# Kernel tuning notes

Hardware: AMD Instinct MI355X
Metric: run time of the kernel (lower is better)

## Reference

```python
import jax, jax.numpy as jnp
import numpy as np

H = 1024
NH = 16
DH = H // NH
EPS = 1e-12


def _heads(x):
    # [B,T,H] -> [B,NH,T,DH]
    B, T, _ = x.shape
    return x.reshape(B, T, NH, DH).transpose(0, 2, 1, 3)


def _layernorm(x, g, b):
    mu = jnp.mean(x, axis=-1, keepdims=True)
    var = jnp.mean(jnp.square(x - mu), axis=-1, keepdims=True)
    return (x - mu) * jax.lax.rsqrt(var + EPS) * g + b


def setup_inputs() -> dict:
    key = jax.random.key(0)
    ks = jax.random.split(key, 24)
    B, Tw, Te = 4, 1024, 128
    s = 0.02
    inp = {
        "word_hidden_states": jax.random.normal(ks[0], (B, Tw, H), jnp.float32),
        "entity_hidden_states": jax.random.normal(ks[1], (B, Te, H), jnp.float32),
        "attention_mask": jnp.zeros((B, 1, 1, Tw + Te), jnp.float32),
        "query_pos": jax.random.normal(ks[2], (B, Te, H), jnp.float32),
    }
    names = ["Wq", "Wk", "Wv", "Weq", "Wek", "Wev", "Wo", "Weo"]
    for i, n in enumerate(names):
        inp[n] = jax.random.normal(ks[3 + i], (H, H), jnp.float32) * s
        inp["b" + n[1:]] = jnp.zeros((H,), jnp.float32)
    inp["ln_g"] = jnp.ones((H,), jnp.float32)
    inp["ln_b"] = jnp.zeros((H,), jnp.float32)
    inp["eln_g"] = jnp.ones((H,), jnp.float32)
    inp["eln_b"] = jnp.zeros((H,), jnp.float32)
    return inp


def reference(word_hidden_states, entity_hidden_states, attention_mask, query_pos,
              Wq, bq, Wk, bk, Wv, bv, Weq, beq, Wek, bek, Wev, bev,
              Wo, bo, Weo, beo, ln_g, ln_b, eln_g, eln_b):
    Tw = word_hidden_states.shape[1]
    pos_ent = (entity_hidden_states + query_pos) * 0.5

    # per-stream projections (entity stream has its own e2w projections)
    qw = _heads(word_hidden_states @ Wq + bq)      # [B,NH,Tw,DH]
    qe = _heads(pos_ent @ Weq + beq)               # [B,NH,Te,DH]
    kw = _heads(word_hidden_states @ Wk + bk)
    ke = _heads(pos_ent @ Wek + bek)
    vw = _heads(word_hidden_states @ Wv + bv)
    ve = _heads(entity_hidden_states @ Wev + bev)  # value uses raw entity states

    q = jnp.concatenate([qw, qe], axis=2)          # [B,NH,T,DH]
    k = jnp.concatenate([kw, ke], axis=2)
    v = jnp.concatenate([vw, ve], axis=2)

    scores = jnp.einsum("bhqd,bhkd->bhqk", q, k) / np.sqrt(DH).astype(np.float32)
    scores = scores + attention_mask
    probs = jax.nn.softmax(scores, axis=-1)
    ctx = jnp.einsum("bhqk,bhkd->bhqd", probs, v)  # [B,NH,T,DH]
    B, _, T, _ = ctx.shape
    ctx = ctx.transpose(0, 2, 1, 3).reshape(B, T, H)

    word_self = ctx[:, :Tw, :]
    ent_self = ctx[:, Tw:, :]

    word_out = _layernorm(word_self @ Wo + bo + word_hidden_states, ln_g, ln_b)
    ent_out = _layernorm(ent_self @ Weo + beo + entity_hidden_states, eln_g, eln_b)
    return (word_out, ent_out)
```

## Files before the change

### kernel.cpp

```cpp
#include <hip/hip_runtime.h>
#include <math.h>

#define H_DIM 1024
#define NHEAD 16
#define DHEAD 64
#define T_W 1024
#define T_E 128
#define T_T 1152
#define BATCH 4

typedef __attribute__((ext_vector_type(8))) short s8b;
typedef __attribute__((ext_vector_type(4))) short s4b;
typedef __attribute__((ext_vector_type(4))) float f32x4;

#define LOG2E 1.44269504088896f

__device__ __forceinline__ unsigned short f2bf(float f) {
    unsigned int u = __float_as_uint(f);
    u = (u + 0x7fffu + ((u >> 16) & 1u)) >> 16;
    return (unsigned short)u;
}

__device__ __forceinline__ unsigned int pk_bf16(float a, float b) {
#if __has_builtin(__builtin_amdgcn_cvt_pk_bf16_f32)
    typedef __bf16 bf2 __attribute__((ext_vector_type(2)));
    bf2 r = __builtin_amdgcn_cvt_pk_bf16_f32(a, b);
    return __builtin_bit_cast(unsigned int, r);
#else
    return (unsigned int)f2bf(a) | ((unsigned int)f2bf(b) << 16);
#endif
}

__device__ __forceinline__ float exp2f_fast(float x) {
#if __has_builtin(__builtin_amdgcn_exp2f)
    return __builtin_amdgcn_exp2f(x);
#else
    return exp2f(x);
#endif
}

__device__ __forceinline__ void gld_lds16(const void* g, void* l) {
    __builtin_amdgcn_global_load_lds(
        (const __attribute__((address_space(1))) unsigned int*)g,
        (__attribute__((address_space(3))) unsigned int*)l, 16, 0, 0);
}

struct WPtrs { const float* w[8]; };
__global__ __launch_bounds__(256) void k_prep2(
    const float* __restrict__ word, const float* __restrict__ ent,
    const float* __restrict__ qp, const float* __restrict__ mask,
    unsigned short* __restrict__ word_bf, unsigned short* __restrict__ pe_bf,
    unsigned short* __restrict__ ent_bf, float* __restrict__ mask2,
    WPtrs ws, unsigned short* __restrict__ Wt)
{
    const int bid = blockIdx.x;
    if (bid < 4096) {
        int i = bid * 256 + threadIdx.x;
        float4 v = ((const float4*)word)[i];
        *(uint2*)(word_bf + (size_t)i * 4) =
            make_uint2(pk_bf16(v.x, v.y), pk_bf16(v.z, v.w));
    } else if (bid < 4608) {
        int i = (bid - 4096) * 256 + threadIdx.x;
        float4 a = ((const float4*)ent)[i];
        float4 b = ((const float4*)qp)[i];
        *(uint2*)(ent_bf + (size_t)i * 4) =
            make_uint2(pk_bf16(a.x, a.y), pk_bf16(a.z, a.w));
        *(uint2*)(pe_bf + (size_t)i * 4) =
            make_uint2(pk_bf16((a.x + b.x) * 0.5f, (a.y + b.y) * 0.5f),
                       pk_bf16((a.z + b.z) * 0.5f, (a.w + b.w) * 0.5f));
    } else if (bid < 4626) {
        int i = (bid - 4608) * 256 + threadIdx.x;
        if (i < BATCH * T_T) mask2[i] = mask[i] * LOG2E;
    } else {
        __shared__ float tile[32][33];
        const int id = bid - 4626;
        const int z = id >> 10, rem = id & 1023;
        const int kb = (rem >> 5) * 32, nb = (rem & 31) * 32;
        const float* src = ws.w[z];
        unsigned short* dst = Wt + (size_t)z * H_DIM * H_DIM;
        const int tx = threadIdx.x & 31, ty = threadIdx.x >> 5;
        #pragma unroll
        for (int i = 0; i < 4; i++)
            tile[ty * 4 + i][tx] = src[(size_t)(kb + ty * 4 + i) * H_DIM + nb + tx];
        __syncthreads();
        #pragma unroll
        for (int i = 0; i < 4; i++)
            dst[(size_t)(nb + ty * 4 + i) * H_DIM + kb + tx] =
                f2bf(tile[tx][ty * 4 + i]);
    }
}

struct B6 { const float* b[6]; };
struct O3p { void* o[3]; };


#define STAGE_GEMM(k0, base)                                                     \
    {                                                                            \
        gld_lds16(gA + (k0), &sm[(base) + t * 8]);                               \
        gld_lds16(gA + (size_t)32 * H_DIM + (k0), &sm[(base) + 2048 + t * 8]);   \
        gld_lds16(gB + (k0), &sm[(base) + 4096 + t * 8]);                        \
        gld_lds16(gB + (size_t)32 * H_DIM + (k0), &sm[(base) + 6144 + t * 8]);   \
        gld_lds16(gB + (size_t)64 * H_DIM + (k0), &sm[(base) + 8192 + t * 8]);   \
        gld_lds16(gB + (size_t)96 * H_DIM + (k0), &sm[(base) + 10240 + t * 8]);  \
    }

#define GEMM_KLOOP                                                               \
    STAGE_GEMM(0, 0)                                                             \
    int base = 0;                                                                \
    for (int k0 = 0; k0 < H_DIM; k0 += 64) {                                     \
        __builtin_amdgcn_s_barrier();                    \
        if (k0 + 64 < H_DIM) {                                                   \
            STAGE_GEMM(k0 + 64, base ^ 12288)                                    \
            asm volatile("s_waitcnt vmcnt(6)" ::: "memory");                     \
        } else {                                                                 \
            asm volatile("s_waitcnt vmcnt(0)" ::: "memory");                     \
        }                                                                        \
        __builtin_amdgcn_s_barrier();                  \
        __builtin_amdgcn_sched_barrier(0);                                       \
        _Pragma("unroll")                                                        \
        for (int kk = 0; kk < 2; kk++) {                                         \
            s8b af[2], bfr[4];                                                   \
            _Pragma("unroll")                                                    \
            for (int mt = 0; mt < 2; mt++) {                                     \
                const int r = wm * 32 + mt * 16 + col;                           \
                af[mt] = *(const s8b*)&sm[base + r * 64 +                        \
                                          (((kk * 4 + quad) ^ (r & 7)) * 8)];    \
            }                                                                    \
            _Pragma("unroll")                                                    \
            for (int nt = 0; nt < 4; nt++) {                                     \
                const int r = wn * 64 + nt * 16 + col;                           \
                bfr[nt] = *(const s8b*)&sm[base + 4096 + r * 64 +                \
                                           (((kk * 4 + quad) ^ (r & 7)) * 8)];   \
            }                                                                    \
            __builtin_amdgcn_s_setprio(1);                                       \
            _Pragma("unroll")                                                    \
            for (int mt = 0; mt < 2; mt++)                                       \
                _Pragma("unroll")                                                \
                for (int nt = 0; nt < 4; nt++)                                   \
                    acc[mt][nt] = __builtin_amdgcn_mfma_f32_16x16x32_bf16(       \
                        af[mt], bfr[nt], acc[mt][nt], 0, 0, 0);                  \
            __builtin_amdgcn_s_setprio(0);                                       \
        }                                                                        \
        base ^= 12288;                                                           \
    }

__global__ __launch_bounds__(256) void k_proj(
    const unsigned short* __restrict__ word_bf,
    const unsigned short* __restrict__ pe_bf,
    const unsigned short* __restrict__ ent_bf,
    const unsigned short* __restrict__ Wtbase, B6 biases, O3p outs)
{
    const int z = blockIdx.z;
    const bool isw = blockIdx.y < 64;
    const int Tseq = isw ? T_W : T_E;
    const int toff = isw ? 0 : T_W;
    const int m0 = (isw ? blockIdx.y : (blockIdx.y - 64)) * 64;
    const unsigned short* A = isw ? word_bf : (z == 2 ? ent_bf : pe_bf);
    const int wi = (isw ? 0 : 3) + z;
    const unsigned short* B = Wtbase + (size_t)wi * H_DIM * H_DIM;
    const float* bias = biases.b[wi];
    void* outp = outs.o[z];

    __shared__ unsigned short sm[24576];
    const int t = threadIdx.x;
    const int w = t >> 6, lane = t & 63;
    const int col = lane & 15, quad = lane >> 4;
    const int n0 = blockIdx.x * 128;
    const int wm = w & 1, wn = w >> 1;

    f32x4 acc[2][4] = {};

    const int rs = t >> 3;
    const int gch = (t & 7) ^ (rs & 7);
    const unsigned short* gA = A + (size_t)(m0 + rs) * H_DIM + gch * 8;
    const unsigned short* gB = B + (size_t)(n0 + rs) * H_DIM + gch * 8;

    GEMM_KLOOP

    #pragma unroll
    for (int mt = 0; mt < 2; mt++) {
        const int mg = m0 + wm * 32 + mt * 16 + quad * 4;
        const int b = mg / Tseq, tt = toff + (mg % Tseq);
        #pragma unroll
        for (int nt = 0; nt < 4; nt++) {
            const int ng = n0 + wn * 64 + nt * 16 + col;
            f32x4 c = acc[mt][nt];
            const float bn = bias[ng];
            if (z < 2) {
                unsigned short* out = (unsigned short*)outp;
                #pragma unroll
                for (int r = 0; r < 4; r++)
                    out[((size_t)b * T_T + tt + r) * H_DIM + ng] = f2bf(c[r] + bn);
            } else {
                unsigned short* out = (unsigned short*)outp;
                *(uint2*)(out + ((size_t)b * H_DIM + ng) * T_T + tt) =
                    make_uint2(pk_bf16(c[0] + bn, c[1] + bn),
                               pk_bf16(c[2] + bn, c[3] + bn));
            }
        }
    }
}

__global__ __launch_bounds__(256) void k_gemm_out(
    const unsigned short* __restrict__ ctx,
    const unsigned short* __restrict__ Wt_o, const unsigned short* __restrict__ Wt_eo,
    const float* __restrict__ bo, const float* __restrict__ beo,
    const float* __restrict__ word, const float* __restrict__ ent,
    float* __restrict__ out_word, float* __restrict__ out_ent)
{
    const int blk = blockIdx.x;
    const bool is_word = blk < 512;
    const int lb = is_word ? blk : blk - 512;
    const int m0 = (lb >> 3) * 64, n0 = (lb & 7) * 128;
    const unsigned short* B = is_word ? Wt_o : Wt_eo;
    const float* bias = is_word ? bo : beo;
    const float* resid = is_word ? word : ent;
    float* out = is_word ? out_word : out_ent;
    const int Tseq = is_word ? T_W : T_E;
    const int toff = is_word ? 0 : T_W;

    __shared__ unsigned short sm[24576];
    const int t = threadIdx.x;
    const int w = t >> 6, lane = t & 63;
    const int col = lane & 15, quad = lane >> 4;
    const int wm = w & 1, wn = w >> 1;

    f32x4 acc[2][4] = {};

    const int rs = t >> 3;
    const int gch = (t & 7) ^ (rs & 7);
    const size_t arow = (size_t)(m0 / Tseq) * T_T + toff + (m0 % Tseq) + rs;
    const unsigned short* gA = ctx + arow * H_DIM + gch * 8;
    const unsigned short* gB = B + (size_t)(n0 + rs) * H_DIM + gch * 8;

    GEMM_KLOOP

    #pragma unroll
    for (int mt = 0; mt < 2; mt++) {
        const int mg = m0 + wm * 32 + mt * 16 + quad * 4;
        #pragma unroll
        for (int nt = 0; nt < 4; nt++) {
            const int ng = n0 + wn * 64 + nt * 16 + col;
            f32x4 c = acc[mt][nt];
            const float bn = bias[ng];
            #pragma unroll
            for (int r = 0; r < 4; r++) {
                const size_t idx = (size_t)(mg + r) * H_DIM + ng;
                out[idx] = c[r] + bn + resid[idx];
            }
        }
    }
}

__global__ __launch_bounds__(512) void k_attn(
    const unsigned short* __restrict__ q, const unsigned short* __restrict__ k,
    const unsigned short* __restrict__ vt, const float* __restrict__ mask2,
    unsigned short* __restrict__ ctx)
{
    const int tid = threadIdx.x;
    const int w = tid >> 6, lane = tid & 63;
    const int col = lane & 15, quad = lane >> 4;
    const int bid = blockIdx.x;
    const int bh = ((bid & 7) << 3) | ((bid >> 3) & 7);
    const int q0 = (bid >> 6) * 128 + w * 16;
    const int b = bh >> 4, h = bh & 15;

    __shared__ unsigned short sK[2][64 * 64];
    __shared__ unsigned short sV[2][64 * 64];
    __shared__ __align__(16) unsigned short sP[8][16 * 64];
    unsigned short* sp = &sP[w][0];

    const unsigned short* qp = q + ((size_t)b * T_T + q0) * H_DIM + h * DHEAD;
    const unsigned short* kp = k + (size_t)b * T_T * H_DIM + h * DHEAD;
    const unsigned short* vp = vt + ((size_t)b * H_DIM + h * DHEAD) * T_T;
    const float* mp = mask2 + (size_t)b * T_T;

    const s8b qf0 = *(const s8b*)(qp + (size_t)col * H_DIM + quad * 8);
    const s8b qf1 = *(const s8b*)(qp + (size_t)col * H_DIM + 32 + quad * 8);

    const int rA = tid >> 3;
    const int cA = (tid & 7) ^ (rA & 7);

    const float SC2 = 0.125f * LOG2E;

    f32x4 O[4] = {};
    float l_part = 0.f;

    #define PREFETCH(J0, BUF)                                                        \
        {                                                                            \
            gld_lds16(kp + (size_t)((J0) + rA) * H_DIM + cA * 8,                     \
                      &sK[BUF][0] + tid * 8);                                        \
            gld_lds16(vp + (size_t)rA * T_T + (J0) + cA * 8,                         \
                      &sV[BUF][0] + tid * 8);                                        \
        }

    PREFETCH(0, 0)
    for (int it = 0; it < 18; it++) {
        const int j0 = it * 64;
        __builtin_amdgcn_s_barrier();
        float4 mrow[4];
        #pragma unroll
        for (int kt = 0; kt < 4; kt++)
            mrow[kt] = *(const float4*)(mp + j0 + kt * 16 + quad * 4);
        __builtin_amdgcn_sched_barrier(0);
        if (it < 17) {
            PREFETCH(j0 + 64, (it + 1) & 1)
            asm volatile("s_waitcnt vmcnt(6)" ::: "memory");
        } else {
            asm volatile("s_waitcnt vmcnt(4)" ::: "memory");
        }
        __builtin_amdgcn_s_barrier();
        __builtin_amdgcn_sched_barrier(0);

        const unsigned short* K0 = &sK[it & 1][0];
        const unsigned short* V0 = &sV[it & 1][0];

        float p[16];
        #pragma unroll
        for (int kt = 0; kt < 4; kt++) {
            const int rk = kt * 16 + col;
            const int csw = quad ^ (rk & 7);
            s8b k0f = *(const s8b*)(K0 + rk * 64 + csw * 8);
            s8b k1f = *(const s8b*)(K0 + rk * 64 + (csw ^ 4) * 8);
            f32x4 z = {0.f, 0.f, 0.f, 0.f};
            __builtin_amdgcn_s_setprio(1);
            z = __builtin_amdgcn_mfma_f32_16x16x32_bf16(k0f, qf0, z, 0, 0, 0);
            z = __builtin_amdgcn_mfma_f32_16x16x32_bf16(k1f, qf1, z, 0, 0, 0);
            __builtin_amdgcn_s_setprio(0);
            float mvv[4] = {mrow[kt].x, mrow[kt].y, mrow[kt].z, mrow[kt].w};
            #pragma unroll
            for (int r = 0; r < 4; r++) {
                float pe = exp2f_fast(fmaf(z[r], SC2, mvv[r]));
                p[kt * 4 + r] = pe;
                l_part += pe;
            }
        }

        #pragma unroll
        for (int kt = 0; kt < 4; kt++) {
            const int chunk = 2 * kt + (quad >> 1);
            *(uint2*)(sp + col * 64 + ((chunk ^ (col & 7)) * 8) + (quad & 1) * 4) =
                make_uint2(pk_bf16(p[4 * kt], p[4 * kt + 1]),
                           pk_bf16(p[4 * kt + 2], p[4 * kt + 3]));
        }
        const s8b p0 = *(const s8b*)(sp + col * 64 + ((quad ^ (col & 7)) * 8));
        const s8b p1 = *(const s8b*)(sp + col * 64 + (((4 + quad) ^ (col & 7)) * 8));

        __builtin_amdgcn_s_setprio(1);
        #pragma unroll
        for (int dt = 0; dt < 4; dt++) {
            const int rf = dt * 16 + col;
            const int csw = quad ^ (rf & 7);
            s8b v0 = *(const s8b*)(V0 + rf * 64 + csw * 8);
            s8b v1 = *(const s8b*)(V0 + rf * 64 + (csw ^ 4) * 8);
            O[dt] = __builtin_amdgcn_mfma_f32_16x16x32_bf16(v0, p0, O[dt], 0, 0, 0);
            O[dt] = __builtin_amdgcn_mfma_f32_16x16x32_bf16(v1, p1, O[dt], 0, 0, 0);
        }
        __builtin_amdgcn_s_setprio(0);
    }
    #undef PREFETCH

    float l_c = l_part;
    l_c += __shfl_xor(l_c, 16);
    l_c += __shfl_xor(l_c, 32);
    const float inv = 1.f / l_c;
    unsigned short* ob = ctx + ((size_t)b * T_T + q0 + col) * H_DIM + h * DHEAD;
    #pragma unroll
    for (int dt = 0; dt < 4; dt++) {
        *(uint2*)(ob + dt * 16 + quad * 4) =
            make_uint2(pk_bf16(O[dt][0] * inv, O[dt][1] * inv),
                       pk_bf16(O[dt][2] * inv, O[dt][3] * inv));
    }
}

__global__ __launch_bounds__(256) void k_layernorm(float* __restrict__ x,
                                                   const float* __restrict__ g0,
                                                   const float* __restrict__ b0,
                                                   const float* __restrict__ g1,
                                                   const float* __restrict__ b1)
{
    const int row = blockIdx.x;
    const float* g = row < 4096 ? g0 : g1;
    const float* bta = row < 4096 ? b0 : b1;
    float* p = x + (size_t)row * H_DIM;
    const int t = threadIdx.x;
    float vals[4];
    float s = 0.f, ss = 0.f;
    #pragma unroll
    for (int i = 0; i < 4; i++) {
        float v = p[t + 256 * i];
        vals[i] = v;
        s += v;
        ss += v * v;
    }
    #pragma unroll
    for (int o = 32; o > 0; o >>= 1) {
        s += __shfl_xor(s, o);
        ss += __shfl_xor(ss, o);
    }
    __shared__ float red[2][4];
    const int wid = t >> 6, lane = t & 63;
    if (lane == 0) { red[0][wid] = s; red[1][wid] = ss; }
    __syncthreads();
    s = red[0][0] + red[0][1] + red[0][2] + red[0][3];
    ss = red[1][0] + red[1][1] + red[1][2] + red[1][3];
    float mu = s * (1.0f / H_DIM);
    float var = ss * (1.0f / H_DIM) - mu * mu;
    float r = rsqrtf(var + 1e-12f);
    #pragma unroll
    for (int i = 0; i < 4; i++) {
        int idx = t + 256 * i;
        p[idx] = (vals[i] - mu) * r * g[idx] + bta[idx];
    }
}

extern "C" void kernel_launch(void* const* d_in, const int* in_sizes, int n_in,
                              void* d_out, int out_size, void* d_ws, size_t ws_size,
                              hipStream_t stream) {
    const float* word = (const float*)d_in[0];
    const float* ent  = (const float*)d_in[1];
    const float* mask = (const float*)d_in[2];
    const float* qpos = (const float*)d_in[3];
    const float* Wq  = (const float*)d_in[4];  const float* bq  = (const float*)d_in[5];
    const float* Wk  = (const float*)d_in[6];  const float* bk  = (const float*)d_in[7];
    const float* Wv  = (const float*)d_in[8];  const float* bv  = (const float*)d_in[9];
    const float* Weq = (const float*)d_in[10]; const float* beq = (const float*)d_in[11];
    const float* Wek = (const float*)d_in[12]; const float* bek = (const float*)d_in[13];
    const float* Wev = (const float*)d_in[14]; const float* bev = (const float*)d_in[15];
    const float* Wo  = (const float*)d_in[16]; const float* bo  = (const float*)d_in[17];
    const float* Weo = (const float*)d_in[18]; const float* beo = (const float*)d_in[19];
    const float* ln_g  = (const float*)d_in[20]; const float* ln_b  = (const float*)d_in[21];
    const float* eln_g = (const float*)d_in[22]; const float* eln_b = (const float*)d_in[23];

    char* ws = (char*)d_ws;
    unsigned short* word_bf = (unsigned short*)(ws);
    unsigned short* pe_bf   = (unsigned short*)(ws + 8388608);
    unsigned short* ent_bf  = (unsigned short*)(ws + 9437184);
    float*          mask2   = (float*)(ws + 10466304);
    unsigned short* Wt      = (unsigned short*)(ws + 10485760);
    unsigned short* qb      = (unsigned short*)(ws + 27262976);
    unsigned short* kb      = (unsigned short*)(ws + 36700160);
    unsigned short* vt      = (unsigned short*)(ws + 46137344);
    unsigned short* ctx     = (unsigned short*)(ws + 55574528);

    float* out_word = (float*)d_out;
    float* out_ent  = out_word + 4194304;

    const size_t WSZ = (size_t)H_DIM * H_DIM;
    unsigned short* Wt_o  = Wt + 6 * WSZ;
    unsigned short* Wt_eo = Wt + 7 * WSZ;

    WPtrs wp = {{Wq, Wk, Wv, Weq, Wek, Wev, Wo, Weo}};
    k_prep2<<<dim3(12818), 256, 0, stream>>>(word, ent, qpos, mask,
                                             word_bf, pe_bf, ent_bf, mask2, wp, Wt);

    B6 bb = {{bq, bk, bv, beq, bek, bev}};
    O3p ow = {{qb, kb, vt}};
    k_proj<<<dim3(8, 72, 3), 256, 0, stream>>>(word_bf, pe_bf, ent_bf, Wt, bb, ow);

    k_attn<<<dim3(NHEAD * BATCH * 9), 512, 0, stream>>>(qb, kb, vt, mask2, ctx);

    k_gemm_out<<<dim3(576), 256, 0, stream>>>(ctx, Wt_o, Wt_eo, bo, beo,
                                              word, ent, out_word, out_ent);

    k_layernorm<<<dim3(4608), 256, 0, stream>>>(out_word, ln_g, ln_b, eln_g, eln_b);
}
```

Before: 253.5 us.

## Switch attention to 32x32x16 MFMA with register-shuffled P, 4 waves per block

Rewrites the attention kernel to use 32x32x16 bf16 MFMA tiles, with each of 4 waves owning 32 query rows instead of 8 waves with 16 rows. The probability tile is moved into the B-operand layout by cross-half lane shuffles instead of a round trip through shared memory. This removes the per-wave LDS P buffer and its stores and loads, and uses fewer, larger MFMAs per K/V tile. The cost is fewer waves per block for latency hiding and twice the per-thread global-to-LDS prefetch work.

```diff
diff --git a/kernel.cpp b/kernel.cpp
--- a/kernel.cpp
+++ b/kernel.cpp
@@ -12,6 +12,8 @@
 typedef __attribute__((ext_vector_type(8))) short s8b;
 typedef __attribute__((ext_vector_type(4))) short s4b;
 typedef __attribute__((ext_vector_type(4))) float f32x4;
+typedef __attribute__((ext_vector_type(16))) float f32x16;
+typedef __attribute__((ext_vector_type(4))) unsigned int u32x4;
 
 #define LOG2E 1.44269504088896f
 
@@ -252,62 +254,69 @@
     }
 }
 
-__global__ __launch_bounds__(512) void k_attn(
+__global__ __launch_bounds__(256) void k_attn(
     const unsigned short* __restrict__ q, const unsigned short* __restrict__ k,
     const unsigned short* __restrict__ vt, const float* __restrict__ mask2,
     unsigned short* __restrict__ ctx)
 {
     const int tid = threadIdx.x;
     const int w = tid >> 6, lane = tid & 63;
-    const int col = lane & 15, quad = lane >> 4;
+    const int qc = lane & 31, h = lane >> 5;
     const int bid = blockIdx.x;
     const int bh = ((bid & 7) << 3) | ((bid >> 3) & 7);
-    const int q0 = (bid >> 6) * 128 + w * 16;
-    const int b = bh >> 4, h = bh & 15;
+    const int q0 = (bid >> 6) * 128;
+    const int b = bh >> 4, hd = bh & 15;
 
     __shared__ unsigned short sK[2][64 * 64];
     __shared__ unsigned short sV[2][64 * 64];
-    __shared__ __align__(16) unsigned short sP[8][16 * 64];
-    unsigned short* sp = &sP[w][0];
-
-    const unsigned short* qp = q + ((size_t)b * T_T + q0) * H_DIM + h * DHEAD;
-    const unsigned short* kp = k + (size_t)b * T_T * H_DIM + h * DHEAD;
-    const unsigned short* vp = vt + ((size_t)b * H_DIM + h * DHEAD) * T_T;
+
+    const unsigned short* qp = q + ((size_t)b * T_T + q0 + w * 32) * H_DIM + hd * DHEAD;
+    const unsigned short* kp = k + (size_t)b * T_T * H_DIM + hd * DHEAD;
+    const unsigned short* vp = vt + ((size_t)b * H_DIM + hd * DHEAD) * T_T;
     const float* mp = mask2 + (size_t)b * T_T;
 
-    const s8b qf0 = *(const s8b*)(qp + (size_t)col * H_DIM + quad * 8);
-    const s8b qf1 = *(const s8b*)(qp + (size_t)col * H_DIM + 32 + quad * 8);
-
-    const int rA = tid >> 3;
-    const int cA = (tid & 7) ^ (rA & 7);
+    s8b qf[4];
+    #pragma unroll
+    for (int ds = 0; ds < 4; ds++)
+        qf[ds] = *(const s8b*)(qp + (size_t)qc * H_DIM + ds * 16 + h * 8);
+
+    const int r1 = tid >> 3;
+    const int c1 = (tid & 7) ^ (r1 & 7);
 
     const float SC2 = 0.125f * LOG2E;
 
-    f32x4 O[4] = {};
+    f32x16 O[2] = {};
     float l_part = 0.f;
 
     #define PREFETCH(J0, BUF)                                                        \
         {                                                                            \
-            gld_lds16(kp + (size_t)((J0) + rA) * H_DIM + cA * 8,                     \
+            gld_lds16(kp + (size_t)((J0) + r1) * H_DIM + c1 * 8,                     \
                       &sK[BUF][0] + tid * 8);                                        \
-            gld_lds16(vp + (size_t)rA * T_T + (J0) + cA * 8,                         \
+            gld_lds16(kp + (size_t)((J0) + 32 + r1) * H_DIM + c1 * 8,                \
+                      &sK[BUF][0] + 2048 + tid * 8);                                 \
+            gld_lds16(vp + (size_t)r1 * T_T + (J0) + c1 * 8,                         \
                       &sV[BUF][0] + tid * 8);                                        \
+            gld_lds16(vp + (size_t)(r1 + 32) * T_T + (J0) + c1 * 8,                  \
+                      &sV[BUF][0] + 2048 + tid * 8);                                 \
         }
 
     PREFETCH(0, 0)
     for (int it = 0; it < 18; it++) {
         const int j0 = it * 64;
         __builtin_amdgcn_s_barrier();
-        float4 mrow[4];
-        #pragma unroll
-        for (int kt = 0; kt < 4; kt++)
-            mrow[kt] = *(const float4*)(mp + j0 + kt * 16 + quad * 4);
+        float4 mr[8];
+        #pragma unroll
+        for (int kb = 0; kb < 2; kb++)
+            #pragma unroll
+            for (int g = 0; g < 4; g++)
+                mr[kb * 4 + g] =
+                    *(const float4*)(mp + j0 + kb * 32 + 8 * g + 4 * h);
         __builtin_amdgcn_sched_barrier(0);
         if (it < 17) {
             PREFETCH(j0 + 64, (it + 1) & 1)
-            asm volatile("s_waitcnt vmcnt(6)" ::: "memory");
+            asm volatile("s_waitcnt vmcnt(12)" ::: "memory");
         } else {
-            asm volatile("s_waitcnt vmcnt(4)" ::: "memory");
+            asm volatile("s_waitcnt vmcnt(8)" ::: "memory");
         }
         __builtin_amdgcn_s_barrier();
         __builtin_amdgcn_sched_barrier(0);
@@ -315,61 +324,85 @@
         const unsigned short* K0 = &sK[it & 1][0];
         const unsigned short* V0 = &sV[it & 1][0];
 
-        float p[16];
-        #pragma unroll
-        for (int kt = 0; kt < 4; kt++) {
-            const int rk = kt * 16 + col;
-            const int csw = quad ^ (rk & 7);
-            s8b k0f = *(const s8b*)(K0 + rk * 64 + csw * 8);
-            s8b k1f = *(const s8b*)(K0 + rk * 64 + (csw ^ 4) * 8);
-            f32x4 z = {0.f, 0.f, 0.f, 0.f};
+        #pragma unroll
+        for (int kb = 0; kb < 2; kb++) {
+            f32x16 z = {};
             __builtin_amdgcn_s_setprio(1);
-            z = __builtin_amdgcn_mfma_f32_16x16x32_bf16(k0f, qf0, z, 0, 0, 0);
-            z = __builtin_amdgcn_mfma_f32_16x16x32_bf16(k1f, qf1, z, 0, 0, 0);
+            #pragma unroll
+            for (int ds = 0; ds < 4; ds++) {
+                const int r = kb * 32 + qc;
+                s8b kf = *(const s8b*)&K0[r * 64 +
+                                          (((ds * 2 + h) ^ (r & 7)) * 8)];
+                z = __builtin_amdgcn_mfma_f32_32x32x16_bf16(kf, qf[ds], z, 0, 0, 0);
+            }
             __builtin_amdgcn_s_setprio(0);
-            float mvv[4] = {mrow[kt].x, mrow[kt].y, mrow[kt].z, mrow[kt].w};
-            #pragma unroll
-            for (int r = 0; r < 4; r++) {
-                float pe = exp2f_fast(fmaf(z[r], SC2, mvv[r]));
-                p[kt * 4 + r] = pe;
-                l_part += pe;
+
+            float p[16];
+            #pragma unroll
+            for (int g = 0; g < 4; g++) {
+                float mv[4] = {mr[kb * 4 + g].x, mr[kb * 4 + g].y,
+                               mr[kb * 4 + g].z, mr[kb * 4 + g].w};
+                #pragma unroll
+                for (int r2 = 0; r2 < 4; r2++) {
+                    float pe = exp2f_fast(fmaf(z[g * 4 + r2], SC2, mv[r2]));
+                    p[g * 4 + r2] = pe;
+                    l_part += pe;
+                }
             }
+
+            unsigned pw[8];
+            #pragma unroll
+            for (int i = 0; i < 8; i++)
+                pw[i] = pk_bf16(p[2 * i], p[2 * i + 1]);
+            s8b pb[2];
+            #pragma unroll
+            for (int cl = 0; cl < 2; cl++) {
+                unsigned a  = pw[cl * 4 + 0], bq = pw[cl * 4 + 1];
+                unsigned c  = pw[cl * 4 + 2], d  = pw[cl * 4 + 3];
+                unsigned sa = (unsigned)__shfl_xor((int)a, 32);
+                unsigned sb = (unsigned)__shfl_xor((int)bq, 32);
+                unsigned sc = (unsigned)__shfl_xor((int)c, 32);
+                unsigned sd = (unsigned)__shfl_xor((int)d, 32);
+                unsigned w0 = h ? sc : a;
+                unsigned w1 = h ? sd : bq;
+                unsigned w2 = h ? c  : sa;
+                unsigned w3 = h ? d  : sb;
+                u32x4 uu = {w0, w1, w2, w3};
+                pb[cl] = __builtin_bit_cast(s8b, uu);
+            }
+
+            __builtin_amdgcn_s_setprio(1);
+            #pragma unroll
+            for (int db = 0; db < 2; db++) {
+                #pragma unroll
+                for (int cl = 0; cl < 2; cl++) {
+                    const int kc = kb * 2 + cl;
+                    const int r = db * 32 + qc;
+                    s8b vf = *(const s8b*)&V0[r * 64 +
+                                              (((kc * 2 + h) ^ (r & 7)) * 8)];
+                    O[db] = __builtin_amdgcn_mfma_f32_32x32x16_bf16(
+                        vf, pb[cl], O[db], 0, 0, 0);
+                }
+            }
+            __builtin_amdgcn_s_setprio(0);
         }
-
-        #pragma unroll
-        for (int kt = 0; kt < 4; kt++) {
-            const int chunk = 2 * kt + (quad >> 1);
-            *(uint2*)(sp + col * 64 + ((chunk ^ (col & 7)) * 8) + (quad & 1) * 4) =
-                make_uint2(pk_bf16(p[4 * kt], p[4 * kt + 1]),
-                           pk_bf16(p[4 * kt + 2], p[4 * kt + 3]));
+    }
+    #undef PREFETCH
+
+    float l_c = l_part + __shfl_xor(l_part, 32);
+    const float inv = 1.f / l_c;
+
+    unsigned short* ob = ctx + ((size_t)b * T_T + q0 + w * 32 + qc) * H_DIM
+                         + hd * DHEAD;
+    #pragma unroll
+    for (int db = 0; db < 2; db++) {
+        #pragma unroll
+        for (int g = 0; g < 4; g++) {
+            const int d0 = db * 32 + 8 * g + 4 * h;
+            *(uint2*)(ob + d0) =
+                make_uint2(pk_bf16(O[db][4 * g] * inv, O[db][4 * g + 1] * inv),
+                           pk_bf16(O[db][4 * g + 2] * inv, O[db][4 * g + 3] * inv));
         }
-        const s8b p0 = *(const s8b*)(sp + col * 64 + ((quad ^ (col & 7)) * 8));
-        const s8b p1 = *(const s8b*)(sp + col * 64 + (((4 + quad) ^ (col & 7)) * 8));
-
-        __builtin_amdgcn_s_setprio(1);
-        #pragma unroll
-        for (int dt = 0; dt < 4; dt++) {
-            const int rf = dt * 16 + col;
-            const int csw = quad ^ (rf & 7);
-            s8b v0 = *(const s8b*)(V0 + rf * 64 + csw * 8);
-            s8b v1 = *(const s8b*)(V0 + rf * 64 + (csw ^ 4) * 8);
-            O[dt] = __builtin_amdgcn_mfma_f32_16x16x32_bf16(v0, p0, O[dt], 0, 0, 0);
-            O[dt] = __builtin_amdgcn_mfma_f32_16x16x32_bf16(v1, p1, O[dt], 0, 0, 0);
-        }
-        __builtin_amdgcn_s_setprio(0);
-    }
-    #undef PREFETCH
-
-    float l_c = l_part;
-    l_c += __shfl_xor(l_c, 16);
-    l_c += __shfl_xor(l_c, 32);
-    const float inv = 1.f / l_c;
-    unsigned short* ob = ctx + ((size_t)b * T_T + q0 + col) * H_DIM + h * DHEAD;
-    #pragma unroll
-    for (int dt = 0; dt < 4; dt++) {
-        *(uint2*)(ob + dt * 16 + quad * 4) =
-            make_uint2(pk_bf16(O[dt][0] * inv, O[dt][1] * inv),
-                       pk_bf16(O[dt][2] * inv, O[dt][3] * inv));
     }
 }
 
@@ -458,7 +491,7 @@
     O3p ow = {{qb, kb, vt}};
     k_proj<<<dim3(8, 72, 3), 256, 0, stream>>>(word_bf, pe_bf, ent_bf, Wt, bb, ow);
 
-    k_attn<<<dim3(NHEAD * BATCH * 9), 512, 0, stream>>>(qb, kb, vt, mask2, ctx);
+    k_attn<<<dim3(NHEAD * BATCH * 9), 256, 0, stream>>>(qb, kb, vt, mask2, ctx);
 
     k_gemm_out<<<dim3(576), 256, 0, stream>>>(ctx, Wt_o, Wt_eo, bo, beo,
                                               word, ent, out_word, out_ent);
```

Result: no change. 257.8 us (+1.7%).
